# Kernel tuning notes

Hardware: AMD Instinct MI355X
Metric: run time of the kernel (lower is better)

Reference implementation:

```python
import jax, jax.numpy as jnp
import numpy as np

B, C, H, W = 8, 64, 256, 256


def _conv1x1(x, w, b):
    # x: [B,Cin,H,W], w: [Cout,Cin], b: [Cout]
    return jnp.einsum('bchw,oc->bohw', x, w) + b[None, :, None, None]


def setup_inputs() -> dict:
    key = jax.random.key(0)
    ks = jax.random.split(key, 6)
    return {
        'hs': jax.random.normal(ks[0], (B, C, H, W), jnp.float32),
        'ref_LR': jax.random.normal(ks[1], (B, 9, H, W), jnp.float32),
        'w_first': jax.random.normal(ks[2], (C, 9), jnp.float32) * 0.1,
        'b_first': jax.random.normal(ks[3], (C,), jnp.float32) * 0.1,
        'w_fuse': jax.random.normal(ks[4], (C, 2 * C), jnp.float32) * 0.05,
        'b_fuse': jax.random.normal(ks[5], (C,), jnp.float32) * 0.1,
    }


def reference(hs, ref_LR, w_first, b_first, w_fuse, b_fuse):
    # 1x1 conv + LeakyReLU(0.1) on the 9-channel reference
    ref = jax.nn.leaky_relu(_conv1x1(ref_LR, w_first, b_first), 0.1)  # [B,C,H,W]
    pad = ((0, 0), (0, 0), (1, 1), (1, 1))
    # Per-pixel, per-channel 3x3 windowed dot product of hs-patch and ref-patch
    # == 3x3 box-sum of the elementwise product (both reflect-padded).
    p = jnp.pad(hs, pad, mode='reflect') * jnp.pad(ref, pad, mode='reflect')
    h, w = hs.shape[2], hs.shape[3]
    cross = jnp.zeros_like(hs)
    for dy in range(3):  # fixed 3x3 window, not a data-dim loop
        for dx in range(3):
            cross = cross + p[:, :, dy:dy + h, dx:dx + w]
    att = jax.nn.sigmoid(cross)            # [B,C,H,W]
    fused = jnp.concatenate((att * hs, hs), axis=1)  # [B,2C,H,W]
    return _conv1x1(fused, w_fuse, b_fuse)  # [B,C,H,W]
```

## Files before the change

### kernel.cpp

```cpp
#include <hip/hip_runtime.h>

#define BB 8
#define CC 64
#define HH 256
#define WW 256
#define HW (HH*WW)

typedef __attribute__((ext_vector_type(8))) short bf16x8;
typedef __attribute__((ext_vector_type(4))) float f32x4;
typedef __attribute__((ext_vector_type(2))) float f32x2;

__device__ __forceinline__ int reflect_idx(int v, int n) {
    if (v < 0) v = -v;
    if (v >= n) v = 2*n - 2 - v;
    return v;
}

__device__ __forceinline__ short f2bf(float f) {
    union { float f; unsigned u; } x; x.f = f;
    unsigned r = (x.u + 0x7fffu + ((x.u >> 16) & 1u)) >> 16;
    return (short)r;
}

__device__ __forceinline__ unsigned cvt_pk_bf16(float lo, float hi) {
    unsigned r;
    asm("v_cvt_pk_bf16_f32 %0, %1, %2" : "=v"(r) : "v"(lo), "v"(hi));
    return r;
}

__global__ __launch_bounds__(256, 3)
void corr_v8_kernel(const float* __restrict__ hs,
                    const float* __restrict__ refLR,
                    const float* __restrict__ w_first,
                    const float* __restrict__ b_first,
                    const float* __restrict__ w_fuse,
                    const float* __restrict__ b_fuse,
                    float* __restrict__ out)
{
    __shared__ short s_w[64 * 136];
    __shared__ short s_fused[4][64 * 40];
    __shared__ float s_p01[4][216];
    __shared__ float s_p23[4][216];

    const int t = threadIdx.x;
    const int wv = t >> 6, lane = t & 63;

    const int d = (int)blockIdx.x;
    const int lid = (d & 7) * 256 + (d >> 3);
    const int bx = lid & 15, by = (lid >> 4) & 15, b = lid >> 8;

    #pragma unroll
    for (int rep = 0; rep < 32; ++rep) {
        int idx = t + rep * 256;
        int m = idx >> 7, kp = idx & 127;
        int g = kp >> 5, i = kp & 31;
        int src = (i < 16) ? (g * 16 + i) : (48 + g * 16 + i);
        s_w[m * 136 + kp] = f2bf(w_fuse[m * 128 + src]);
    }
    __syncthreads();

    const int y0 = by * 16 + wv * 4;
    const int x0 = bx * 16;

    const bool has1 = lane < 44;
    int g0, g1;
    {
        const int py = lane / 18, px = lane % 18;
        g0 = reflect_idx(y0 + py - 1, HH) * WW + reflect_idx(x0 + px - 1, WW);
    }
    {
        const int pp = 64 + lane;
        const int py = pp / 18, px = pp % 18;
        const int gt = reflect_idx(y0 + py - 1, HH) * WW + reflect_idx(x0 + px - 1, WW);
        g1 = has1 ? gt : g0;
    }
    const int pyc = lane >> 4, pxc = lane & 15;
    const int gc = (y0 + pyc) * WW + (x0 + pxc);

    const float* rb = refLR + (size_t)b * 9 * HW;
    float rin0[9], rin1[9];
    #pragma unroll
    for (int j = 0; j < 9; ++j) rin0[j] = rb[(size_t)j * HW + g0];
    #pragma unroll
    for (int j = 0; j < 9; ++j) rin1[j] = rb[(size_t)j * HW + g1];

    const int cl = lane & 15, kb = lane >> 4;
    f32x4 acc[4][4];
    #pragma unroll
    for (int mt = 0; mt < 4; ++mt) {
        #pragma unroll
        for (int r = 0; r < 4; ++r) {
            const float bv = b_fuse[mt * 16 + kb * 4 + r];
            #pragma unroll
            for (int nt = 0; nt < 4; ++nt) acc[mt][nt][r] = bv;
        }
    }

    const float* hsb = hs + (size_t)b * CC * HW;
    float* const sp01 = s_p01[wv];
    float* const sp23 = s_p23[wv];
    short* const sfw  = s_fused[wv];
    const int pb = (pyc * 18 + pxc) * 2;

    float h0[4], h1[4], hc[4];
    #pragma unroll
    for (int cc = 0; cc < 4; ++cc) {
        const float* hp = hsb + (size_t)cc * HW;
        h0[cc] = hp[g0]; h1[cc] = hp[g1]; hc[cc] = hp[gc];
    }

    #pragma unroll 1
    for (int ch = 0; ch < 16; ++ch) {
        const int c0 = ch * 4;

        float pr0[4], pr1[4], hcv[4];
        #pragma unroll
        for (int cc = 0; cc < 4; ++cc) {
            const int c = c0 + cc;
            float v0 = b_first[c], v1 = v0;
            #pragma unroll
            for (int j = 0; j < 9; ++j) {
                const float w = w_first[c * 9 + j];
                v0 = fmaf(w, rin0[j], v0);
                v1 = fmaf(w, rin1[j], v1);
            }
            v0 = v0 > 0.f ? v0 : 0.1f * v0;
            v1 = v1 > 0.f ? v1 : 0.1f * v1;
            pr0[cc] = h0[cc] * v0;
            pr1[cc] = h1[cc] * v1;
            hcv[cc] = hc[cc];
        }
        *(f32x2*)&sp01[lane * 2] = (f32x2){pr0[0], pr0[1]};
        *(f32x2*)&sp23[lane * 2] = (f32x2){pr0[2], pr0[3]};
        if (has1) {
            *(f32x2*)&sp01[(64 + lane) * 2] = (f32x2){pr1[0], pr1[1]};
            *(f32x2*)&sp23[(64 + lane) * 2] = (f32x2){pr1[2], pr1[3]};
        }
        asm volatile("s_waitcnt lgkmcnt(0)" ::: "memory");

        f32x2 a01 = (f32x2){0.f, 0.f}, a23 = (f32x2){0.f, 0.f};
        #pragma unroll
        for (int dy = 0; dy < 3; ++dy)
            #pragma unroll
            for (int dx = 0; dx < 3; ++dx) {
                const int o = pb + (dy * 18 + dx) * 2;
                a01 += *(const f32x2*)&sp01[o];
                a23 += *(const f32x2*)&sp23[o];
            }

        {
            const int cn = ((ch + 1) & 15) * 4;
            #pragma unroll
            for (int cc = 0; cc < 4; ++cc) {
                const float* hp = hsb + (size_t)(cn + cc) * HW;
                h0[cc] = hp[g0]; h1[cc] = hp[g1]; hc[cc] = hp[gc];
            }
        }

        const float cr[4] = {a01[0], a01[1], a23[0], a23[1]};
        float av[4];
        #pragma unroll
        for (int cc = 0; cc < 4; ++cc)
            av[cc] = __builtin_amdgcn_rcpf(
                1.0f + __builtin_amdgcn_exp2f(cr[cc] * -1.44269504088896f)) * hcv[cc];
        uint2 ua, uh;
        ua.x = cvt_pk_bf16(av[0], av[1]);
        ua.y = cvt_pk_bf16(av[2], av[3]);
        uh.x = cvt_pk_bf16(hcv[0], hcv[1]);
        uh.y = cvt_pk_bf16(hcv[2], hcv[3]);
        const int k4 = (ch & 3) * 4;
        *(uint2*)&sfw[lane * 40 + k4]      = ua;
        *(uint2*)&sfw[lane * 40 + 16 + k4] = uh;

        if ((ch & 3) == 3) {
            asm volatile("s_waitcnt lgkmcnt(0)" ::: "memory");
            const int g = ch >> 2;
            #pragma unroll
            for (int nt = 0; nt < 4; ++nt) {
                const bf16x8 bf = *(const bf16x8*)&sfw[(nt * 16 + cl) * 40 + kb * 8];
                #pragma unroll
                for (int mt = 0; mt < 4; ++mt) {
                    const bf16x8 af = *(const bf16x8*)&s_w[(mt * 16 + cl) * 136 + g * 32 + kb * 8];
                    acc[mt][nt] = __builtin_amdgcn_mfma_f32_16x16x32_bf16(af, bf, acc[mt][nt], 0, 0, 0);
                }
            }
        }
    }

    float* const ob = out + (size_t)b * CC * HW;
    #pragma unroll
    for (int mt = 0; mt < 4; ++mt) {
        #pragma unroll
        for (int nt = 0; nt < 4; ++nt) {
            #pragma unroll
            for (int r = 0; r < 4; ++r) {
                const int o = mt * 16 + kb * 4 + r;
                ob[(size_t)o * HW + (size_t)(y0 + nt) * WW + (x0 + cl)] = acc[mt][nt][r];
            }
        }
    }
}

extern "C" void kernel_launch(void* const* d_in, const int* in_sizes, int n_in,
                              void* d_out, int out_size, void* d_ws, size_t ws_size,
                              hipStream_t stream) {
    const float* hs      = (const float*)d_in[0];
    const float* refLR   = (const float*)d_in[1];
    const float* w_first = (const float*)d_in[2];
    const float* b_first = (const float*)d_in[3];
    const float* w_fuse  = (const float*)d_in[4];
    const float* b_fuse  = (const float*)d_in[5];
    float* out = (float*)d_out;

    corr_v8_kernel<<<dim3(2048), dim3(256), 0, stream>>>(hs, refLR, w_first, b_first,
                                                         w_fuse, b_fuse, out);
}
```

Measured before the change: 106.3 us.

## Precompute bf16 MFMA weight fragments in a prep kernel and drop shared weight tile

A small one-block prep kernel now converts w_fuse to bf16 and writes it straight into the per-lane MFMA A-fragment layout in workspace. The main kernel no longer stages a 17KB shared weight tile with a block-wide sync; it loads each group's fragments from global (L2-resident) into registers just before the MFMA step. Launch bounds rise from 3 to 5 blocks per CU, which the smaller LDS footprint permits. The cost is an extra kernel launch, global fragment loads every four channel iterations, and more register pressure under the tighter occupancy bound.

```diff
diff --git a/kernel.cpp b/kernel.cpp
--- a/kernel.cpp
+++ b/kernel.cpp
@@ -28,16 +28,36 @@
     return r;
 }
 
-__global__ __launch_bounds__(256, 3)
-void corr_v8_kernel(const float* __restrict__ hs,
+__global__ void corr_prep_kernel(const float* __restrict__ w_fuse,
+                                 bf16x8* __restrict__ afbuf) {
+    const int t = threadIdx.x;
+    const int lane = t & 63;
+    #pragma unroll
+    for (int pass = 0; pass < 4; ++pass) {
+        const int combo = (t >> 6) + pass * 4;
+        const int g = combo >> 2, mt = combo & 3;
+        const int m = mt * 16 + (lane & 15);
+        const int kb = lane >> 4;
+        bf16x8 v;
+        #pragma unroll
+        for (int j = 0; j < 8; ++j) {
+            const int i = kb * 8 + j;
+            const int src = (i < 16) ? (g * 16 + i) : (48 + g * 16 + i);
+            v[j] = f2bf(w_fuse[m * 128 + src]);
+        }
+        afbuf[combo * 64 + lane] = v;
+    }
+}
+
+__global__ __launch_bounds__(256, 5)
+void corr_v9_kernel(const float* __restrict__ hs,
                     const float* __restrict__ refLR,
                     const float* __restrict__ w_first,
                     const float* __restrict__ b_first,
-                    const float* __restrict__ w_fuse,
+                    const bf16x8* __restrict__ afbuf,
                     const float* __restrict__ b_fuse,
                     float* __restrict__ out)
 {
-    __shared__ short s_w[64 * 136];
     __shared__ short s_fused[4][64 * 40];
     __shared__ float s_p01[4][216];
     __shared__ float s_p23[4][216];
@@ -48,16 +68,6 @@
     const int d = (int)blockIdx.x;
     const int lid = (d & 7) * 256 + (d >> 3);
     const int bx = lid & 15, by = (lid >> 4) & 15, b = lid >> 8;
-
-    #pragma unroll
-    for (int rep = 0; rep < 32; ++rep) {
-        int idx = t + rep * 256;
-        int m = idx >> 7, kp = idx & 127;
-        int g = kp >> 5, i = kp & 31;
-        int src = (i < 16) ? (g * 16 + i) : (48 + g * 16 + i);
-        s_w[m * 136 + kp] = f2bf(w_fuse[m * 128 + src]);
-    }
-    __syncthreads();
 
     const int y0 = by * 16 + wv * 4;
     const int x0 = bx * 16;
@@ -112,6 +122,14 @@
     #pragma unroll 1
     for (int ch = 0; ch < 16; ++ch) {
         const int c0 = ch * 4;
+
+        bf16x8 af[4];
+        if ((ch & 3) == 3) {
+            const int g = ch >> 2;
+            #pragma unroll
+            for (int mt = 0; mt < 4; ++mt)
+                af[mt] = afbuf[(g * 4 + mt) * 64 + lane];
+        }
 
         float pr0[4], pr1[4], hcv[4];
         #pragma unroll
@@ -174,15 +192,12 @@
 
         if ((ch & 3) == 3) {
             asm volatile("s_waitcnt lgkmcnt(0)" ::: "memory");
-            const int g = ch >> 2;
             #pragma unroll
             for (int nt = 0; nt < 4; ++nt) {
                 const bf16x8 bf = *(const bf16x8*)&sfw[(nt * 16 + cl) * 40 + kb * 8];
                 #pragma unroll
-                for (int mt = 0; mt < 4; ++mt) {
-                    const bf16x8 af = *(const bf16x8*)&s_w[(mt * 16 + cl) * 136 + g * 32 + kb * 8];
-                    acc[mt][nt] = __builtin_amdgcn_mfma_f32_16x16x32_bf16(af, bf, acc[mt][nt], 0, 0, 0);
-                }
+                for (int mt = 0; mt < 4; ++mt)
+                    acc[mt][nt] = __builtin_amdgcn_mfma_f32_16x16x32_bf16(af[mt], bf, acc[mt][nt], 0, 0, 0);
             }
         }
     }
@@ -211,7 +226,9 @@
     const float* w_fuse  = (const float*)d_in[4];
     const float* b_fuse  = (const float*)d_in[5];
     float* out = (float*)d_out;
-
-    corr_v8_kernel<<<dim3(2048), dim3(256), 0, stream>>>(hs, refLR, w_first, b_first,
-                                                         w_fuse, b_fuse, out);
-}
+    bf16x8* afbuf = (bf16x8*)d_ws;
+
+    corr_prep_kernel<<<dim3(1), dim3(256), 0, stream>>>(w_fuse, afbuf);
+    corr_v9_kernel<<<dim3(2048), dim3(256), 0, stream>>>(hs, refLR, w_first, b_first,
+                                                         afbuf, b_fuse, out);
+}
```

Result: slower. 368.6 us (+246.9%).

## Software-pipeline box-sum with double-buffered LDS and two-ahead hs prefetch

Applied to the files above, without the earlier changes.

Splits the per-wave product buffer into two ping-pong LDS buffers. Each chunk's product tile is computed and stored one iteration ahead, so the box-sum reads of the current chunk overlap with the stores and math for the next. The hs loads are prefetched two chunks ahead, the weight fragments are loaded before the MFMA step, and the explicit lgkmcnt waits are removed. This costs more registers and LDS, which could lower occupancy under the launch bounds of 3 blocks. It also relies on wave-local ordering instead of explicit waits, so the correctness of the LDS hazards depends on the compiler inserting the needed waits.

```diff
diff --git a/kernel.cpp b/kernel.cpp
--- a/kernel.cpp
+++ b/kernel.cpp
@@ -29,18 +29,17 @@
 }
 
 __global__ __launch_bounds__(256, 3)
-void corr_v8_kernel(const float* __restrict__ hs,
-                    const float* __restrict__ refLR,
-                    const float* __restrict__ w_first,
-                    const float* __restrict__ b_first,
-                    const float* __restrict__ w_fuse,
-                    const float* __restrict__ b_fuse,
-                    float* __restrict__ out)
+void corr_v11_kernel(const float* __restrict__ hs,
+                     const float* __restrict__ refLR,
+                     const float* __restrict__ w_first,
+                     const float* __restrict__ b_first,
+                     const float* __restrict__ w_fuse,
+                     const float* __restrict__ b_fuse,
+                     float* __restrict__ out)
 {
     __shared__ short s_w[64 * 136];
     __shared__ short s_fused[4][64 * 40];
-    __shared__ float s_p01[4][216];
-    __shared__ float s_p23[4][216];
+    __shared__ float s_pd[4][2][432];
 
     const int t = threadIdx.x;
     const int wv = t >> 6, lane = t & 63;
@@ -97,30 +96,24 @@
     }
 
     const float* hsb = hs + (size_t)b * CC * HW;
-    float* const sp01 = s_p01[wv];
-    float* const sp23 = s_p23[wv];
-    short* const sfw  = s_fused[wv];
+    short* const sfw = s_fused[wv];
     const int pb = (pyc * 18 + pxc) * 2;
 
-    float h0[4], h1[4], hc[4];
+    float h0[4], h1[4], hcC[4], hcN[4];
     #pragma unroll
     for (int cc = 0; cc < 4; ++cc) {
         const float* hp = hsb + (size_t)cc * HW;
-        h0[cc] = hp[g0]; h1[cc] = hp[g1]; hc[cc] = hp[gc];
-    }
-
-    #pragma unroll 1
-    for (int ch = 0; ch < 16; ++ch) {
-        const int c0 = ch * 4;
-
-        float pr0[4], pr1[4], hcv[4];
+        h0[cc] = hp[g0]; h1[cc] = hp[g1]; hcC[cc] = hp[gc];
+    }
+    {
+        float* const pw = s_pd[wv][0];
+        float pr0[4], pr1[4];
         #pragma unroll
         for (int cc = 0; cc < 4; ++cc) {
-            const int c = c0 + cc;
-            float v0 = b_first[c], v1 = v0;
+            float v0 = b_first[cc], v1 = v0;
             #pragma unroll
             for (int j = 0; j < 9; ++j) {
-                const float w = w_first[c * 9 + j];
+                const float w = w_first[cc * 9 + j];
                 v0 = fmaf(w, rin0[j], v0);
                 v1 = fmaf(w, rin1[j], v1);
             }
@@ -128,63 +121,116 @@
             v1 = v1 > 0.f ? v1 : 0.1f * v1;
             pr0[cc] = h0[cc] * v0;
             pr1[cc] = h1[cc] * v1;
-            hcv[cc] = hc[cc];
-        }
-        *(f32x2*)&sp01[lane * 2] = (f32x2){pr0[0], pr0[1]};
-        *(f32x2*)&sp23[lane * 2] = (f32x2){pr0[2], pr0[3]};
+        }
+        *(f32x2*)&pw[lane * 2]       = (f32x2){pr0[0], pr0[1]};
+        *(f32x2*)&pw[216 + lane * 2] = (f32x2){pr0[2], pr0[3]};
         if (has1) {
-            *(f32x2*)&sp01[(64 + lane) * 2] = (f32x2){pr1[0], pr1[1]};
-            *(f32x2*)&sp23[(64 + lane) * 2] = (f32x2){pr1[2], pr1[3]};
-        }
-        asm volatile("s_waitcnt lgkmcnt(0)" ::: "memory");
-
-        f32x2 a01 = (f32x2){0.f, 0.f}, a23 = (f32x2){0.f, 0.f};
+            *(f32x2*)&pw[(64 + lane) * 2]       = (f32x2){pr1[0], pr1[1]};
+            *(f32x2*)&pw[216 + (64 + lane) * 2] = (f32x2){pr1[2], pr1[3]};
+        }
+    }
+    #pragma unroll
+    for (int cc = 0; cc < 4; ++cc) {
+        const float* hp = hsb + (size_t)(4 + cc) * HW;
+        h0[cc] = hp[g0]; h1[cc] = hp[g1]; hcN[cc] = hp[gc];
+    }
+
+    float* prd = s_pd[wv][0];
+    float* pw  = s_pd[wv][1];
+
+    #pragma unroll 1
+    for (int ch = 0; ch < 16; ++ch) {
+        bf16x8 af[4];
+        if ((ch & 3) == 3) {
+            const int g = ch >> 2;
+            #pragma unroll
+            for (int mt = 0; mt < 4; ++mt)
+                af[mt] = *(const bf16x8*)&s_w[(mt * 16 + cl) * 136 + g * 32 + kb * 8];
+        }
+
+        f32x2 rb01[9], rb23[9];
         #pragma unroll
         for (int dy = 0; dy < 3; ++dy)
             #pragma unroll
             for (int dx = 0; dx < 3; ++dx) {
                 const int o = pb + (dy * 18 + dx) * 2;
-                a01 += *(const f32x2*)&sp01[o];
-                a23 += *(const f32x2*)&sp23[o];
-            }
-
-        {
-            const int cn = ((ch + 1) & 15) * 4;
+                rb01[dy * 3 + dx] = *(const f32x2*)&prd[o];
+                rb23[dy * 3 + dx] = *(const f32x2*)&prd[216 + o];
+            }
+
+        if (ch < 15) {
+            const int c0 = (ch + 1) * 4;
+            float pr0[4], pr1[4];
             #pragma unroll
             for (int cc = 0; cc < 4; ++cc) {
-                const float* hp = hsb + (size_t)(cn + cc) * HW;
-                h0[cc] = hp[g0]; h1[cc] = hp[g1]; hc[cc] = hp[gc];
-            }
-        }
-
+                const int c = c0 + cc;
+                float v0 = b_first[c], v1 = v0;
+                #pragma unroll
+                for (int j = 0; j < 9; ++j) {
+                    const float w = w_first[c * 9 + j];
+                    v0 = fmaf(w, rin0[j], v0);
+                    v1 = fmaf(w, rin1[j], v1);
+                }
+                v0 = v0 > 0.f ? v0 : 0.1f * v0;
+                v1 = v1 > 0.f ? v1 : 0.1f * v1;
+                pr0[cc] = h0[cc] * v0;
+                pr1[cc] = h1[cc] * v1;
+            }
+            *(f32x2*)&pw[lane * 2]       = (f32x2){pr0[0], pr0[1]};
+            *(f32x2*)&pw[216 + lane * 2] = (f32x2){pr0[2], pr0[3]};
+            if (has1) {
+                *(f32x2*)&pw[(64 + lane) * 2]       = (f32x2){pr1[0], pr1[1]};
+                *(f32x2*)&pw[216 + (64 + lane) * 2] = (f32x2){pr1[2], pr1[3]};
+            }
+        }
+
+        f32x2 a01 = rb01[0], a23 = rb23[0];
+        #pragma unroll
+        for (int j = 1; j < 9; ++j) { a01 += rb01[j]; a23 += rb23[j]; }
         const float cr[4] = {a01[0], a01[1], a23[0], a23[1]};
         float av[4];
         #pragma unroll
         for (int cc = 0; cc < 4; ++cc)
             av[cc] = __builtin_amdgcn_rcpf(
-                1.0f + __builtin_amdgcn_exp2f(cr[cc] * -1.44269504088896f)) * hcv[cc];
+                1.0f + __builtin_amdgcn_exp2f(cr[cc] * -1.44269504088896f)) * hcC[cc];
+
         uint2 ua, uh;
         ua.x = cvt_pk_bf16(av[0], av[1]);
         ua.y = cvt_pk_bf16(av[2], av[3]);
-        uh.x = cvt_pk_bf16(hcv[0], hcv[1]);
-        uh.y = cvt_pk_bf16(hcv[2], hcv[3]);
+        uh.x = cvt_pk_bf16(hcC[0], hcC[1]);
+        uh.y = cvt_pk_bf16(hcC[2], hcC[3]);
         const int k4 = (ch & 3) * 4;
         *(uint2*)&sfw[lane * 40 + k4]      = ua;
         *(uint2*)&sfw[lane * 40 + 16 + k4] = uh;
 
         if ((ch & 3) == 3) {
-            asm volatile("s_waitcnt lgkmcnt(0)" ::: "memory");
-            const int g = ch >> 2;
             #pragma unroll
             for (int nt = 0; nt < 4; ++nt) {
                 const bf16x8 bf = *(const bf16x8*)&sfw[(nt * 16 + cl) * 40 + kb * 8];
                 #pragma unroll
-                for (int mt = 0; mt < 4; ++mt) {
-                    const bf16x8 af = *(const bf16x8*)&s_w[(mt * 16 + cl) * 136 + g * 32 + kb * 8];
-                    acc[mt][nt] = __builtin_amdgcn_mfma_f32_16x16x32_bf16(af, bf, acc[mt][nt], 0, 0, 0);
-                }
-            }
-        }
+                for (int mt = 0; mt < 4; ++mt)
+                    acc[mt][nt] = __builtin_amdgcn_mfma_f32_16x16x32_bf16(af[mt], bf, acc[mt][nt], 0, 0, 0);
+            }
+        }
+
+        if (ch < 14) {
+            const int cn = (ch + 2) * 4;
+            #pragma unroll
+            for (int cc = 0; cc < 4; ++cc) {
+                const float* hp = hsb + (size_t)(cn + cc) * HW;
+                h0[cc] = hp[g0]; h1[cc] = hp[g1];
+            }
+        }
+        #pragma unroll
+        for (int cc = 0; cc < 4; ++cc) hcC[cc] = hcN[cc];
+        if (ch < 14) {
+            const int cn = (ch + 2) * 4;
+            #pragma unroll
+            for (int cc = 0; cc < 4; ++cc)
+                hcN[cc] = hsb[(size_t)(cn + cc) * HW + gc];
+        }
+
+        float* tmp = prd; prd = pw; pw = tmp;
     }
 
     float* const ob = out + (size_t)b * CC * HW;
@@ -212,6 +258,6 @@
     const float* b_fuse  = (const float*)d_in[5];
     float* out = (float*)d_out;
 
-    corr_v8_kernel<<<dim3(2048), dim3(256), 0, stream>>>(hs, refLR, w_first, b_first,
-                                                         w_fuse, b_fuse, out);
-}
+    corr_v11_kernel<<<dim3(2048), dim3(256), 0, stream>>>(hs, refLR, w_first, b_first,
+                                                          w_fuse, b_fuse, out);
+}
```

Result: slower. 298.1 us (+180.5%).
